# Kernel optimization log

Measured on AMD Instinct MI355X. Metric: run time of the kernel, lower is better.

## Reference

```python
import jax, jax.numpy as jnp
import numpy as np

R = 256   # resolution
C = 16    # n_chan
F = 8     # n_freq
N = 262144


def setup_inputs() -> dict:
    key = jax.random.key(0)
    k1, k2 = jax.random.split(key)
    coords = jax.random.uniform(k1, (N, 3), dtype=jnp.float32, minval=-1.0, maxval=1.0)
    grid = jax.random.normal(k2, (3, C * F, R, R), dtype=jnp.float32) * 0.1
    # matches torch init: linspace(0,1,C*F).reshape(-1,C).T.reshape(-1)
    freqs = jnp.linspace(0.0, 1.0, C * F, dtype=jnp.float32).reshape(-1, C).T.reshape(-1)
    return {"coords": coords, "grid": grid, "freqs": freqs}


def _reflect(x, size):
    # PyTorch grid_sample reflection padding, align_corners=True:
    # reflect unnormalized coords about [0, size-1], period 2*(size-1)
    span = size - 1
    m = 2 * span
    r = jnp.abs(x) % m
    return jnp.where(r > span, m - r, r)


def _grid_sample_plane(img, xy):
    # img: (CF, R, R); xy: (Npts, 2) normalized [-1,1], (x indexes W, y indexes H)
    ix = _reflect((xy[:, 0] + 1.0) * 0.5 * (R - 1), R)
    iy = _reflect((xy[:, 1] + 1.0) * 0.5 * (R - 1), R)
    x0f = jnp.floor(ix); y0f = jnp.floor(iy)
    wx = ix - x0f; wy = iy - y0f
    x0 = jnp.clip(x0f.astype(jnp.int32), 0, R - 1)
    x1 = jnp.clip(x0 + 1, 0, R - 1)
    y0 = jnp.clip(y0f.astype(jnp.int32), 0, R - 1)
    y1 = jnp.clip(y0 + 1, 0, R - 1)
    v00 = img[:, y0, x0]  # (CF, Npts)
    v01 = img[:, y0, x1]
    v10 = img[:, y1, x0]
    v11 = img[:, y1, x1]
    return (v00 * (1 - wx) * (1 - wy) + v01 * wx * (1 - wy)
            + v10 * (1 - wx) * wy + v11 * wx * wy)


def reference(coords, grid, freqs):
    n = coords.shape[0]
    # tri-plane sample coords: plane0 (y,z), plane1 (x,z), plane2 (x,y)
    xy = jnp.stack([coords[:, (1, 2)], coords[:, (0, 2)], coords[:, (0, 1)]], 0)  # (3,N,2)
    coefs = jax.vmap(_grid_sample_plane)(grid, xy)          # (3, CF, N)
    coefs = coefs.transpose(2, 1, 0).reshape(n, C, F, 3)    # (N, C, F, 3)
    # get_freqs(): 2**(clamp(freqs,0,1)*log2(R)) - 1
    fr = 2.0 ** (jnp.clip(freqs, 0.0, 1.0) * np.float32(np.log2(R))) - 1.0  # (CF,)
    pts = (coords + 1.0) * 0.5 * (R - 1)                    # (N, 3)
    phase = (jnp.pi / R) * (pts[:, None, None, :] + 0.5) * (fr.reshape(C, F)[None, :, :, None] + 0.5)
    basis = jnp.cos(phase)                                   # (N, C, F, 3)
    # einsum BCFT,BCFT->BCT then sum over T == sum over (F, T)
    return 2.0 * jnp.sum(coefs * basis, axis=(2, 3))         # (N, C)
```

## Files before the change

kernel.cpp:

```cpp
#include <hip/hip_runtime.h>

#define RES 256
#define NCH 128
#define NC  16
#define QG  32
#define NPK 64

__device__ __forceinline__ unsigned int f32_to_bf16_rne(float f) {
    unsigned int u = __float_as_uint(f);
    return (u + 0x7FFFu + ((u >> 16) & 1u)) >> 16;
}
__device__ __forceinline__ float bf16_lo(unsigned int w) {
    return __uint_as_float(w << 16);
}
__device__ __forceinline__ float bf16_hi(unsigned int w) {
    return __uint_as_float(w & 0xFFFF0000u);
}

__global__ __launch_bounds__(256) void fg_transpose_bf16(
    const float* __restrict__ in, unsigned int* __restrict__ out)
{
    __shared__ float tile[QG][RES + 1];
    const int tid = threadIdx.x;
    const int qg = blockIdx.x;
    const int y  = blockIdx.y;
    const int p  = blockIdx.z;
    const int q0 = qg * QG;

    const float* src = in + (((size_t)p * NCH + q0) * RES + y) * RES;
    #pragma unroll
    for (int it = 0; it < (QG * RES) / 256; ++it) {
        const int lin = it * 256 + tid;
        const int qq = lin >> 8;
        const int x  = lin & 255;
        tile[qq][x] = src[(size_t)qq * (RES * RES) + x];
    }
    __syncthreads();
    unsigned int* dst = out + (((size_t)p * RES + y) * RES) * NPK + (q0 >> 1);
    #pragma unroll
    for (int it = 0; it < (RES * (QG / 2)) / 256; ++it) {
        const int lin = it * 256 + tid;
        const int qp = lin & 15;
        const int x  = lin >> 4;
        const unsigned int lo = f32_to_bf16_rne(tile[2 * qp + 0][x]);
        const unsigned int hi = f32_to_bf16_rne(tile[2 * qp + 1][x]);
        dst[(size_t)x * NPK + qp] = lo | (hi << 16);
    }
}

__device__ __forceinline__ float reflectf(float v) {
    float r = fabsf(v);
    r = fmodf(r, 510.0f);
    return (r > 255.0f) ? (510.0f - r) : r;
}

__global__ __launch_bounds__(256) void fg_main_bf16(
    const float* __restrict__ coords,
    const unsigned int* __restrict__ grid,
    const float* __restrict__ freqs,
    float* __restrict__ out, int n)
{
    const int t = threadIdx.x;
    const int c = t & 15;
    const int i = blockIdx.x * 16 + (t >> 4);
    if (i >= n) return;

    float frp[8];
    #pragma unroll
    for (int j = 0; j < 8; ++j) {
        float f = fminf(fmaxf(freqs[c * 8 + j], 0.0f), 1.0f);
        frp[j] = __builtin_amdgcn_exp2f(f * 8.0f) - 0.5f;
    }

    const float c0 = coords[3 * (size_t)i + 0];
    const float c1 = coords[3 * (size_t)i + 1];
    const float c2 = coords[3 * (size_t)i + 2];
    const float pts0 = (c0 + 1.0f) * 127.5f;
    const float pts1 = (c1 + 1.0f) * 127.5f;
    const float pts2 = (c2 + 1.0f) * 127.5f;

    float acc = 0.0f;

    #pragma unroll
    for (int p = 0; p < 3; ++p) {
        const float sx = (p == 0) ? pts1 : pts0;
        const float sy = (p == 2) ? pts1 : pts2;
        const float pp = (p == 0) ? pts0 : ((p == 1) ? pts1 : pts2);

        const float ix = reflectf(sx);
        const float iy = reflectf(sy);
        const float x0f = floorf(ix), y0f = floorf(iy);
        const float wx = ix - x0f, wy = iy - y0f;
        int x0 = (int)x0f; x0 = min(max(x0, 0), RES - 1);
        int y0 = (int)y0f; y0 = min(max(y0, 0), RES - 1);
        const int x1 = min(x0 + 1, RES - 1);
        const int y1 = min(y0 + 1, RES - 1);
        const float w00 = (1.0f - wx) * (1.0f - wy);
        const float w01 = wx * (1.0f - wy);
        const float w10 = (1.0f - wx) * wy;
        const float w11 = wx * wy;
        const float A = (pp + 0.5f) * (1.0f / 512.0f);

        const size_t rowbase = ((size_t)p * RES) * RES;
        const unsigned int* b00 = grid + (rowbase + (size_t)y0 * RES + x0) * NPK + c * 4;
        const unsigned int* b01 = grid + (rowbase + (size_t)y0 * RES + x1) * NPK + c * 4;
        const unsigned int* b10 = grid + (rowbase + (size_t)y1 * RES + x0) * NPK + c * 4;
        const unsigned int* b11 = grid + (rowbase + (size_t)y1 * RES + x1) * NPK + c * 4;
        const uint4 g00 = *(const uint4*)b00;
        const uint4 g01 = *(const uint4*)b01;
        const uint4 g10 = *(const uint4*)b10;
        const uint4 g11 = *(const uint4*)b11;
        const unsigned int w0[4] = {g00.x, g00.y, g00.z, g00.w};
        const unsigned int w1[4] = {g01.x, g01.y, g01.z, g01.w};
        const unsigned int w2[4] = {g10.x, g10.y, g10.z, g10.w};
        const unsigned int w3[4] = {g11.x, g11.y, g11.z, g11.w};

        #pragma unroll
        for (int jj = 0; jj < 4; ++jj) {
            const float clo = w00 * bf16_lo(w0[jj]) + w01 * bf16_lo(w1[jj])
                            + w10 * bf16_lo(w2[jj]) + w11 * bf16_lo(w3[jj]);
            const float chi = w00 * bf16_hi(w0[jj]) + w01 * bf16_hi(w1[jj])
                            + w10 * bf16_hi(w2[jj]) + w11 * bf16_hi(w3[jj]);
            const float rl = __builtin_amdgcn_fractf(A * frp[2 * jj + 0]);
            const float rh = __builtin_amdgcn_fractf(A * frp[2 * jj + 1]);
            acc += clo * __builtin_amdgcn_cosf(rl);
            acc += chi * __builtin_amdgcn_cosf(rh);
        }
    }

    out[(size_t)i * NC + c] = 2.0f * acc;
}

__global__ __launch_bounds__(256) void fg_main_f32(
    const float* __restrict__ coords,
    const float* __restrict__ grid,
    const float* __restrict__ freqs,
    float* __restrict__ out, int n)
{
    const int t = threadIdx.x;
    const int c = t & 15;
    const int i = blockIdx.x * 16 + (t >> 4);
    if (i >= n) return;

    float frp[8];
    #pragma unroll
    for (int j = 0; j < 8; ++j) {
        float f = fminf(fmaxf(freqs[c * 8 + j], 0.0f), 1.0f);
        frp[j] = __builtin_amdgcn_exp2f(f * 8.0f) - 0.5f;
    }
    const float c0 = coords[3 * (size_t)i + 0];
    const float c1 = coords[3 * (size_t)i + 1];
    const float c2 = coords[3 * (size_t)i + 2];
    const float pts0 = (c0 + 1.0f) * 127.5f;
    const float pts1 = (c1 + 1.0f) * 127.5f;
    const float pts2 = (c2 + 1.0f) * 127.5f;
    float acc = 0.0f;
    #pragma unroll
    for (int p = 0; p < 3; ++p) {
        const float sx = (p == 0) ? pts1 : pts0;
        const float sy = (p == 2) ? pts1 : pts2;
        const float pp = (p == 0) ? pts0 : ((p == 1) ? pts1 : pts2);
        const float ix = reflectf(sx);
        const float iy = reflectf(sy);
        const float x0f = floorf(ix), y0f = floorf(iy);
        const float wx = ix - x0f, wy = iy - y0f;
        int x0 = (int)x0f; x0 = min(max(x0, 0), RES - 1);
        int y0 = (int)y0f; y0 = min(max(y0, 0), RES - 1);
        const int x1 = min(x0 + 1, RES - 1);
        const int y1 = min(y0 + 1, RES - 1);
        const float w00 = (1.0f - wx) * (1.0f - wy);
        const float w01 = wx * (1.0f - wy);
        const float w10 = (1.0f - wx) * wy;
        const float w11 = wx * wy;
        const float A = (pp + 0.5f) * (1.0f / 512.0f);
        const size_t plane = (size_t)p * NCH * RES * RES;
        const int o00 = y0 * RES + x0, o01 = y0 * RES + x1;
        const int o10 = y1 * RES + x0, o11 = y1 * RES + x1;
        #pragma unroll
        for (int j = 0; j < 8; ++j) {
            const float* gq = grid + plane + (size_t)(c * 8 + j) * (RES * RES);
            const float coef = w00 * gq[o00] + w01 * gq[o01]
                             + w10 * gq[o10] + w11 * gq[o11];
            const float rr = __builtin_amdgcn_fractf(A * frp[j]);
            acc += coef * __builtin_amdgcn_cosf(rr);
        }
    }
    out[(size_t)i * NC + c] = 2.0f * acc;
}

extern "C" void kernel_launch(void* const* d_in, const int* in_sizes, int n_in,
                              void* d_out, int out_size, void* d_ws, size_t ws_size,
                              hipStream_t stream)
{
    const float* coords = (const float*)d_in[0];
    const float* grid   = (const float*)d_in[1];
    const float* freqs  = (const float*)d_in[2];
    float* out = (float*)d_out;
    const int n = in_sizes[0] / 3;

    const size_t tbytes = (size_t)3 * RES * RES * NPK * sizeof(unsigned int);
    const int blocks = (n + 15) / 16;

    if (ws_size >= tbytes) {
        unsigned int* gridT = (unsigned int*)d_ws;
        hipLaunchKernelGGL(fg_transpose_bf16, dim3(4, RES, 3), dim3(256), 0, stream,
                           grid, gridT);
        hipLaunchKernelGGL(fg_main_bf16, dim3(blocks), dim3(256), 0, stream,
                           coords, gridT, freqs, out, n);
    } else {
        hipLaunchKernelGGL(fg_main_f32, dim3(blocks), dim3(256), 0, stream,
                           coords, grid, freqs, out, n);
    }
}
```

Before: 271.6 us.

## Sort points by Morton cell before sampling to improve grid cache locality

Adds a counting sort of points into 4096 Morton-ordered 3D cells (histogram, scan, scatter kernels), then the main kernel processes points in sorted order through a permutation so neighbouring threads touch nearby grid texels. The transpose kernel now loads with float4 vectors, and the frequency transform is precomputed once in the scan kernel. The aim is to cut cache misses on the random bilinear gathers, at the cost of three extra launches, a memset, atomics, and scattered output writes.

```diff
diff --git a/kernel.cpp b/kernel.cpp
--- a/kernel.cpp
+++ b/kernel.cpp
@@ -1,10 +1,11 @@
 #include <hip/hip_runtime.h>
 
-#define RES 256
-#define NCH 128
-#define NC  16
-#define QG  32
-#define NPK 64
+#define RES   256
+#define NCH   128
+#define NC    16
+#define QG    32
+#define NPK   64
+#define NBINS 4096
 
 __device__ __forceinline__ unsigned int f32_to_bf16_rne(float f) {
     unsigned int u = __float_as_uint(f);
@@ -16,11 +17,28 @@
 __device__ __forceinline__ float bf16_hi(unsigned int w) {
     return __uint_as_float(w & 0xFFFF0000u);
 }
+__device__ __forceinline__ float reflectf(float v) {
+    float r = fabsf(v);
+    r = fmodf(r, 510.0f);
+    return (r > 255.0f) ? (510.0f - r) : r;
+}
+__device__ __forceinline__ unsigned spread3(unsigned v) {
+    return (v & 1u) | ((v & 2u) << 2) | ((v & 4u) << 4) | ((v & 8u) << 6);
+}
+__device__ __forceinline__ int point_cell(const float* __restrict__ coords, int i) {
+    const float r0 = reflectf((coords[3 * (size_t)i + 0] + 1.0f) * 127.5f);
+    const float r1 = reflectf((coords[3 * (size_t)i + 1] + 1.0f) * 127.5f);
+    const float r2 = reflectf((coords[3 * (size_t)i + 2] + 1.0f) * 127.5f);
+    const unsigned cx = (unsigned)min(max((int)r0, 0), 255) >> 4;
+    const unsigned cy = (unsigned)min(max((int)r1, 0), 255) >> 4;
+    const unsigned cz = (unsigned)min(max((int)r2, 0), 255) >> 4;
+    return (int)(spread3(cx) | (spread3(cy) << 1) | (spread3(cz) << 2));
+}
 
 __global__ __launch_bounds__(256) void fg_transpose_bf16(
     const float* __restrict__ in, unsigned int* __restrict__ out)
 {
-    __shared__ float tile[QG][RES + 1];
+    __shared__ float tile[QG][RES + 4];
     const int tid = threadIdx.x;
     const int qg = blockIdx.x;
     const int y  = blockIdx.y;
@@ -29,11 +47,12 @@
 
     const float* src = in + (((size_t)p * NCH + q0) * RES + y) * RES;
     #pragma unroll
-    for (int it = 0; it < (QG * RES) / 256; ++it) {
+    for (int it = 0; it < (QG * RES / 4) / 256; ++it) {
         const int lin = it * 256 + tid;
-        const int qq = lin >> 8;
-        const int x  = lin & 255;
-        tile[qq][x] = src[(size_t)qq * (RES * RES) + x];
+        const int qq = lin >> 6;
+        const int x4 = lin & 63;
+        *(float4*)&tile[qq][x4 * 4] =
+            *(const float4*)(src + (size_t)qq * (RES * RES) + x4 * 4);
     }
     __syncthreads();
     unsigned int* dst = out + (((size_t)p * RES + y) * RES) * NPK + (q0 >> 1);
@@ -48,29 +67,67 @@
     }
 }
 
-__device__ __forceinline__ float reflectf(float v) {
-    float r = fabsf(v);
-    r = fmodf(r, 510.0f);
-    return (r > 255.0f) ? (510.0f - r) : r;
+__global__ __launch_bounds__(256) void fg_hist(
+    const float* __restrict__ coords, unsigned* __restrict__ hist, int n)
+{
+    const int i = blockIdx.x * 256 + threadIdx.x;
+    if (i >= n) return;
+    atomicAdd(&hist[point_cell(coords, i)], 1u);
+}
+
+__global__ __launch_bounds__(256) void fg_scan(
+    const unsigned* __restrict__ hist, unsigned* __restrict__ cursor,
+    const float* __restrict__ freqs, float* __restrict__ frp)
+{
+    __shared__ unsigned s[256];
+    const int t = threadIdx.x;
+    unsigned loc[16];
+    unsigned sum = 0;
+    #pragma unroll
+    for (int k = 0; k < 16; ++k) { loc[k] = hist[t * 16 + k]; sum += loc[k]; }
+    s[t] = sum;
+    __syncthreads();
+    for (int off = 1; off < 256; off <<= 1) {
+        unsigned v = (t >= off) ? s[t - off] : 0u;
+        __syncthreads();
+        s[t] += v;
+        __syncthreads();
+    }
+    unsigned base = (t == 0) ? 0u : s[t - 1];
+    #pragma unroll
+    for (int k = 0; k < 16; ++k) { cursor[t * 16 + k] = base; base += loc[k]; }
+    if (t < 128) {
+        const float f = fminf(fmaxf(freqs[t], 0.0f), 1.0f);
+        frp[t] = __builtin_amdgcn_exp2f(f * 8.0f) - 0.5f;
+    }
+}
+
+__global__ __launch_bounds__(256) void fg_scatter(
+    const float* __restrict__ coords, unsigned* __restrict__ cursor,
+    unsigned* __restrict__ perm, int n)
+{
+    const int i = blockIdx.x * 256 + threadIdx.x;
+    if (i >= n) return;
+    const unsigned pos = atomicAdd(&cursor[point_cell(coords, i)], 1u);
+    perm[pos] = (unsigned)i;
 }
 
 __global__ __launch_bounds__(256) void fg_main_bf16(
     const float* __restrict__ coords,
     const unsigned int* __restrict__ grid,
-    const float* __restrict__ freqs,
+    const float* __restrict__ frp_in,
+    const unsigned* __restrict__ perm,
     float* __restrict__ out, int n)
 {
     const int t = threadIdx.x;
     const int c = t & 15;
-    const int i = blockIdx.x * 16 + (t >> 4);
-    if (i >= n) return;
+    const int slot = blockIdx.x * 16 + (t >> 4);
+    if (slot >= n) return;
+    const int i = (int)perm[slot];
 
     float frp[8];
-    #pragma unroll
-    for (int j = 0; j < 8; ++j) {
-        float f = fminf(fmaxf(freqs[c * 8 + j], 0.0f), 1.0f);
-        frp[j] = __builtin_amdgcn_exp2f(f * 8.0f) - 0.5f;
-    }
+    *(float4*)(frp + 0) = *(const float4*)(frp_in + c * 8 + 0);
+    *(float4*)(frp + 4) = *(const float4*)(frp_in + c * 8 + 4);
 
     const float c0 = coords[3 * (size_t)i + 0];
     const float c1 = coords[3 * (size_t)i + 1];
@@ -198,15 +255,33 @@
     float* out = (float*)d_out;
     const int n = in_sizes[0] / 3;
 
-    const size_t tbytes = (size_t)3 * RES * RES * NPK * sizeof(unsigned int);
+    const size_t gridT_b  = (size_t)3 * RES * RES * NPK * sizeof(unsigned);
+    const size_t hist_b   = (size_t)NBINS * sizeof(unsigned);
+    const size_t frp_b    = 128 * sizeof(float);
+    const size_t perm_b   = (size_t)((n + 3) & ~3) * sizeof(unsigned);
+    const size_t need = gridT_b + 2 * hist_b + frp_b + perm_b;
+
     const int blocks = (n + 15) / 16;
 
-    if (ws_size >= tbytes) {
-        unsigned int* gridT = (unsigned int*)d_ws;
+    if (ws_size >= need) {
+        char* ws = (char*)d_ws;
+        unsigned* gridT  = (unsigned*)ws;                 ws += gridT_b;
+        unsigned* hist   = (unsigned*)ws;                 ws += hist_b;
+        unsigned* cursor = (unsigned*)ws;                 ws += hist_b;
+        float*    frp    = (float*)ws;                    ws += frp_b;
+        unsigned* perm   = (unsigned*)ws;
+
+        hipMemsetAsync(hist, 0, hist_b, stream);
+        hipLaunchKernelGGL(fg_hist, dim3((n + 255) / 256), dim3(256), 0, stream,
+                           coords, hist, n);
+        hipLaunchKernelGGL(fg_scan, dim3(1), dim3(256), 0, stream,
+                           hist, cursor, freqs, frp);
+        hipLaunchKernelGGL(fg_scatter, dim3((n + 255) / 256), dim3(256), 0, stream,
+                           coords, cursor, perm, n);
         hipLaunchKernelGGL(fg_transpose_bf16, dim3(4, RES, 3), dim3(256), 0, stream,
                            grid, gridT);
         hipLaunchKernelGGL(fg_main_bf16, dim3(blocks), dim3(256), 0, stream,
-                           coords, gridT, freqs, out, n);
+                           coords, gridT, frp, perm, out, n);
     } else {
         hipLaunchKernelGGL(fg_main_f32, dim3(blocks), dim3(256), 0, stream,
                            coords, grid, freqs, out, n);
```

New measurement: 288.9 us. 6.3% more time.
